# Kernel tuning notes

Hardware: AMD Instinct MI355X
Metric: run time of the kernel (lower is better)

The kernel has to match this reference:

```python
import jax, jax.numpy as jnp
import numpy as np
from jax import lax

H = 2048          # hidden_size
I = 1408          # moe_intermediate_size
E = 16            # n_routed_experts
K = 4             # num_experts_per_tok
N_SHARED = 2      # n_shared_experts
IS = I * N_SHARED # shared expert intermediate
B, S = 1, 1024


def setup_inputs() -> dict:
    key = jax.random.key(0)
    ks = jax.random.split(key, 8)
    scale = 0.02
    return {
        "hidden_states": jax.random.normal(ks[0], (B, S, H), dtype=jnp.float32),
        "gate_w": jax.random.normal(ks[1], (E, H), dtype=jnp.float32) * scale,  # MoEGate.weight
        "w_gate": jax.random.normal(ks[2], (E, H, I), dtype=jnp.float32) * scale,
        "w_up": jax.random.normal(ks[3], (E, H, I), dtype=jnp.float32) * scale,
        "w_down": jax.random.normal(ks[4], (E, I, H), dtype=jnp.float32) * scale,
        "sw_gate": jax.random.normal(ks[5], (H, IS), dtype=jnp.float32) * scale,
        "sw_up": jax.random.normal(ks[6], (H, IS), dtype=jnp.float32) * scale,
        "sw_down": jax.random.normal(ks[7], (IS, H), dtype=jnp.float32) * scale,
    }


def _moe_forward(hidden_states, gate_w, w_gate, w_up, w_down, sw_gate, sw_up, sw_down):
    bsz, seq_len, h = hidden_states.shape
    flat = hidden_states.reshape(-1, h)                # [T, H]
    T = flat.shape[0]

    # --- MoEGate: softmax scoring + top-k (norm_topk_prob=False) ---
    logits = flat @ gate_w.T                           # [T, E]
    scores = jax.nn.softmax(logits, axis=-1)
    topk_w, topk_idx = lax.top_k(scores, K)            # [T, K]

    # combine[t, e] = sum of top-k weights assigned to expert e (scatter of dispatch)
    combine = jnp.zeros((T, E), dtype=flat.dtype).at[
        jnp.arange(T)[:, None], topk_idx
    ].add(topk_w)                                      # [T, E]

    # --- routed experts: scan over experts, accumulate weighted SwiGLU MLP outputs ---
    def step(y, xs):
        wg, wu, wd, c = xs                             # [H,I], [H,I], [I,H], [T]
        out = (jax.nn.silu(flat @ wg) * (flat @ wu)) @ wd   # [T, H]
        return y + c[:, None] * out, None

    y, _ = lax.scan(step, jnp.zeros_like(flat), (w_gate, w_up, w_down, combine.T))

    # --- shared experts (always-on SwiGLU MLP with larger intermediate) ---
    shared = (jax.nn.silu(flat @ sw_gate) * (flat @ sw_up)) @ sw_down  # [T, H]

    return (y + shared).reshape(bsz, seq_len, h)


def reference(hidden_states, gate_w, w_gate, w_up, w_down, sw_gate, sw_up, sw_down):
    return _moe_forward(hidden_states, gate_w, w_gate, w_up, w_down,
                        sw_gate, sw_up, sw_down)
```

## Files before the change

kernel.cpp:

```cpp
#include <hip/hip_runtime.h>
#include <hip/hip_bf16.h>
#include <stdint.h>

#define T_TOK 1024
#define H_DIM 2048
#define I_DIM 1408
#define E_NUM 16
#define K_TOP 4
#define IS_DIM 2816
#define BK 64
#define BKP 72
#define BM 128
#define BN 128
#define NT_MAX 64

typedef __hip_bfloat16 bf;
typedef __attribute__((ext_vector_type(8))) __bf16 bf16x8;
typedef __attribute__((ext_vector_type(4))) float f32x4;

__device__ __forceinline__ void gload16(const void* g, void* l) {
  __builtin_amdgcn_global_load_lds((const __attribute__((address_space(1))) void*)g,
                                   (__attribute__((address_space(3))) void*)l, 16, 0, 0);
}

__global__ void cvt_x_kernel(const float* __restrict__ in, bf* __restrict__ out) {
  int i = blockIdx.x * blockDim.x + threadIdx.x;
  float4 v = reinterpret_cast<const float4*>(in)[i];
  int b = i * 4;
  out[b + 0] = __float2bfloat16(v.x);
  out[b + 1] = __float2bfloat16(v.y);
  out[b + 2] = __float2bfloat16(v.z);
  out[b + 3] = __float2bfloat16(v.w);
}

__global__ void gate_topk_kernel(const float* __restrict__ x, const float* __restrict__ gw,
                                 int* __restrict__ topk_idx, float* __restrict__ topk_w) {
  int t = blockIdx.x;
  int lane = threadIdx.x;
  float acc[E_NUM];
#pragma unroll
  for (int e = 0; e < E_NUM; e++) acc[e] = 0.f;
  const float* xt = x + (long)t * H_DIM;
  for (int h = lane; h < H_DIM; h += 64) {
    float xv = xt[h];
#pragma unroll
    for (int e = 0; e < E_NUM; e++) acc[e] += xv * gw[e * H_DIM + h];
  }
#pragma unroll
  for (int e = 0; e < E_NUM; e++) {
    float v = acc[e];
    for (int off = 32; off; off >>= 1) v += __shfl_xor(v, off, 64);
    acc[e] = v;
  }
  if (lane == 0) {
    float m = acc[0];
#pragma unroll
    for (int e = 1; e < E_NUM; e++) m = fmaxf(m, acc[e]);
    float sc[E_NUM];
    float s = 0.f;
#pragma unroll
    for (int e = 0; e < E_NUM; e++) { sc[e] = expf(acc[e] - m); s += sc[e]; }
    float inv = 1.f / s;
#pragma unroll
    for (int e = 0; e < E_NUM; e++) sc[e] *= inv;
    for (int k = 0; k < K_TOP; k++) {
      int bi = 0;
      float bv = sc[0];
      for (int e = 1; e < E_NUM; e++)
        if (sc[e] > bv) { bv = sc[e]; bi = e; }
      topk_idx[t * K_TOP + k] = bi;
      topk_w[t * K_TOP + k] = bv;
      sc[bi] = -1.f;
    }
  }
}

__global__ void build_lists_kernel(const int* __restrict__ topk_idx,
                                   int* __restrict__ rows, int* __restrict__ tile_expert,
                                   int* __restrict__ n_tiles) {
  __shared__ int cnt[E_NUM], cur[E_NUM], s_tb;
  int tid = threadIdx.x;
  if (tid < E_NUM) cnt[tid] = 0;
  __syncthreads();
  for (int p = tid; p < T_TOK * K_TOP; p += blockDim.x)
    atomicAdd(&cnt[topk_idx[p]], 1);
  __syncthreads();
  if (tid == 0) {
    int tb = 0;
    for (int e = 0; e < E_NUM; e++) {
      int nt = (cnt[e] + BM - 1) / BM;
      cur[e] = tb * BM;
      for (int j = 0; j < nt; j++) tile_expert[tb + j] = e;
      tb += nt;
    }
    for (int j = 0; j < 16; j++) tile_expert[tb + j] = 16 + (j >> 3);
    s_tb = tb;
    *n_tiles = tb + 16;
  }
  __syncthreads();
  int tb = s_tb;
  for (int r = tid; r < NT_MAX * BM; r += blockDim.x) rows[r] = -1;
  __syncthreads();
  for (int p = tid; p < T_TOK * K_TOP; p += blockDim.x) {
    int t = p >> 2, k = p & 3;
    int e = topk_idx[p];
    int slot = atomicAdd(&cur[e], 1);
    rows[slot] = t * 8 + k;
  }
  for (int idx = tid; idx < 16 * BM; idx += blockDim.x) {
    int j = idx >> 7, r = idx & 127;
    int t = (j & 7) * BM + r;
    rows[(tb + j) * BM + r] = t * 8 + 4 + (j >> 3);
  }
}

__launch_bounds__(256, 2)
__global__ void gemm_gateup_kernel(const bf* __restrict__ xb,
                                   const int* __restrict__ rows,
                                   const int* __restrict__ tile_expert,
                                   const int* __restrict__ n_tiles,
                                   const float* __restrict__ Wg,
                                   const float* __restrict__ Wu,
                                   const float* __restrict__ SWg,
                                   const float* __restrict__ SWu,
                                   bf* __restrict__ act) {
  int bid = blockIdx.x;
  const int q = (11 * NT_MAX) / 8;
  int idx = (bid & 7) * q + (bid >> 3);
  int x = idx / NT_MAX, rt = idx % NT_MAX;
  if (rt >= *n_tiles) return;
  int e = tile_expert[rt];
  bool sh = e >= 16;
  const float* gbase = sh ? (SWg + (e - 16) * I_DIM) : (Wg + (long)e * H_DIM * I_DIM);
  const float* ubase = sh ? (SWu + (e - 16) * I_DIM) : (Wu + (long)e * H_DIM * I_DIM);
  long bstride = sh ? IS_DIM : I_DIM;
  int i0 = x * BN;

  __shared__ bf lA[BM * BK];
  __shared__ bf lG[BN * BKP];
  __shared__ bf lU[BN * BKP];

  int tid = threadIdx.x, w = tid >> 6, lane = tid & 63;
  int l15 = lane & 15, lhi = lane >> 4;
  int kg = tid >> 5, ng = tid & 31;
  int sswz = (((lane & 7) ^ (lane >> 3)) * 8);
  int bco = (kg ^ (ng & 7)) * 8;

  const bf* asrc[4];
#pragma unroll
  for (int i = 0; i < 4; i++) {
    int rr = rt * BM + i * 32 + w * 8 + (lane >> 3);
    int p = rows[rr];
    int tok = (p >= 0) ? (p >> 3) : 0;
    asrc[i] = xb + (long)tok * H_DIM + sswz;
  }

  const float* pg = gbase + i0 + ng * 4 + (long)(kg * 8) * bstride;
  const float* pu = ubase + i0 + ng * 4 + (long)(kg * 8) * bstride;

  f32x4 accg[4][4], accu[4][4];
  f32x4 z4 = {0.f, 0.f, 0.f, 0.f};
#pragma unroll
  for (int m = 0; m < 4; m++)
#pragma unroll
    for (int n = 0; n < 4; n++) { accg[m][n] = z4; accu[m][n] = z4; }

  int wr = w >> 1, wc = w & 1;
  for (int kt = 0; kt < H_DIM; kt += BK) {
    float4 vg[8], vu[8];
    const float* pgk = pg + (long)kt * bstride;
    const float* puk = pu + (long)kt * bstride;
#pragma unroll
    for (int j = 0; j < 8; j++) {
      vg[j] = *reinterpret_cast<const float4*>(pgk + (long)j * bstride);
      vu[j] = *reinterpret_cast<const float4*>(puk + (long)j * bstride);
    }
    __syncthreads();
#pragma unroll
    for (int i = 0; i < 4; i++)
      gload16(asrc[i] + kt, lA + (i * 32 + w * 8) * BK);
#pragma unroll
    for (int c = 0; c < 4; c++) {
      union { bf16x8 v; bf s[8]; } og, ou;
#pragma unroll
      for (int j = 0; j < 8; j++) {
        og.s[j] = __float2bfloat16(((const float*)&vg[j])[c]);
        ou.s[j] = __float2bfloat16(((const float*)&vu[j])[c]);
      }
      *reinterpret_cast<bf16x8*>(lG + (ng * 4 + c) * BKP + bco) = og.v;
      *reinterpret_cast<bf16x8*>(lU + (ng * 4 + c) * BKP + bco) = ou.v;
    }
    __syncthreads();
#pragma unroll
    for (int kk = 0; kk < 2; kk++) {
      bf16x8 af[4];
#pragma unroll
      for (int m = 0; m < 4; m++)
        af[m] = *reinterpret_cast<const bf16x8*>(
            lA + (wr * 64 + m * 16 + l15) * BK + (((kk * 4 + lhi) ^ (l15 & 7)) * 8));
#pragma unroll
      for (int n = 0; n < 4; n++) {
        int nrow = wc * 64 + n * 16 + l15;
        int bch = ((kk * 4 + lhi) ^ ((nrow >> 2) & 7)) * 8;
        bf16x8 gf = *reinterpret_cast<const bf16x8*>(lG + nrow * BKP + bch);
        bf16x8 uf = *reinterpret_cast<const bf16x8*>(lU + nrow * BKP + bch);
#pragma unroll
        for (int m = 0; m < 4; m++) {
          accg[m][n] = __builtin_amdgcn_mfma_f32_16x16x32_bf16(af[m], gf, accg[m][n], 0, 0, 0);
          accu[m][n] = __builtin_amdgcn_mfma_f32_16x16x32_bf16(af[m], uf, accu[m][n], 0, 0, 0);
        }
      }
    }
  }

#pragma unroll
  for (int m = 0; m < 4; m++)
#pragma unroll
    for (int n = 0; n < 4; n++)
#pragma unroll
      for (int r2 = 0; r2 < 4; r2++) {
        float gv = accg[m][n][r2];
        float uv = accu[m][n][r2];
        float s = (gv / (1.f + __expf(-gv))) * uv;
        int row = rt * BM + wr * 64 + m * 16 + lhi * 4 + r2;
        int col = i0 + wc * 64 + n * 16 + l15;
        act[(long)row * I_DIM + col] = __float2bfloat16(s);
      }
}

__launch_bounds__(256, 3)
__global__ void gemm_down_kernel(const bf* __restrict__ A,
                                 const int* __restrict__ rows,
                                 const int* __restrict__ tile_expert,
                                 const int* __restrict__ n_tiles,
                                 const float* __restrict__ Wd,
                                 const float* __restrict__ SWd,
                                 bf* __restrict__ outp) {
  int bid = blockIdx.x;
  const int q = (16 * NT_MAX) / 8;
  int idx = (bid & 7) * q + (bid >> 3);
  int x = idx / NT_MAX, rt = idx % NT_MAX;
  if (rt >= *n_tiles) return;
  int e = tile_expert[rt];
  bool sh = e >= 16;
  const float* bbase = sh ? (SWd + (long)(e - 16) * I_DIM * H_DIM)
                          : (Wd + (long)e * I_DIM * H_DIM);
  int h0 = x * BN;

  __shared__ bf lA[BM * BK];
  __shared__ bf lB[BN * BKP];
  __shared__ int rowsl[BM];

  int tid = threadIdx.x, w = tid >> 6, lane = tid & 63;
  int l15 = lane & 15, lhi = lane >> 4;
  int kg = tid >> 5, ng = tid & 31;
  int sswz = (((lane & 7) ^ (lane >> 3)) * 8);
  int bco = (kg ^ (ng & 7)) * 8;
  if (tid < BM) rowsl[tid] = rows[rt * BM + tid];

  long aoff[4];
#pragma unroll
  for (int i = 0; i < 4; i++)
    aoff[i] = (long)(rt * BM + i * 32 + w * 8 + (lane >> 3)) * I_DIM + sswz;

  const float* pb = bbase + h0 + ng * 4 + (long)(kg * 8) * H_DIM;

  f32x4 acc[4][4];
  f32x4 z4 = {0.f, 0.f, 0.f, 0.f};
#pragma unroll
  for (int m = 0; m < 4; m++)
#pragma unroll
    for (int n = 0; n < 4; n++) acc[m][n] = z4;

  int wr = w >> 1, wc = w & 1;
  for (int kt = 0; kt < I_DIM; kt += BK) {
    float4 vb[8];
    const float* pbk = pb + (long)kt * H_DIM;
#pragma unroll
    for (int j = 0; j < 8; j++)
      vb[j] = *reinterpret_cast<const float4*>(pbk + (long)j * H_DIM);
    __syncthreads();
#pragma unroll
    for (int i = 0; i < 4; i++)
      gload16(A + aoff[i] + kt, lA + (i * 32 + w * 8) * BK);
#pragma unroll
    for (int c = 0; c < 4; c++) {
      union { bf16x8 v; bf s[8]; } ob;
#pragma unroll
      for (int j = 0; j < 8; j++)
        ob.s[j] = __float2bfloat16(((const float*)&vb[j])[c]);
      *reinterpret_cast<bf16x8*>(lB + (ng * 4 + c) * BKP + bco) = ob.v;
    }
    __syncthreads();
#pragma unroll
    for (int kk = 0; kk < 2; kk++) {
      bf16x8 af[4];
#pragma unroll
      for (int m = 0; m < 4; m++)
        af[m] = *reinterpret_cast<const bf16x8*>(
            lA + (wr * 64 + m * 16 + l15) * BK + (((kk * 4 + lhi) ^ (l15 & 7)) * 8));
#pragma unroll
      for (int n = 0; n < 4; n++) {
        int nrow = wc * 64 + n * 16 + l15;
        int bch = ((kk * 4 + lhi) ^ ((nrow >> 2) & 7)) * 8;
        bf16x8 bfr = *reinterpret_cast<const bf16x8*>(lB + nrow * BKP + bch);
#pragma unroll
        for (int m = 0; m < 4; m++)
          acc[m][n] = __builtin_amdgcn_mfma_f32_16x16x32_bf16(af[m], bfr, acc[m][n], 0, 0, 0);
      }
    }
  }

#pragma unroll
  for (int m = 0; m < 4; m++)
#pragma unroll
    for (int n = 0; n < 4; n++)
#pragma unroll
      for (int r2 = 0; r2 < 4; r2++) {
        int lrow = wr * 64 + m * 16 + lhi * 4 + r2;
        int col = h0 + wc * 64 + n * 16 + l15;
        int p = rowsl[lrow];
        if (p >= 0) outp[(long)p * H_DIM + col] = __float2bfloat16(acc[m][n][r2]);
      }
}

__global__ void combine_kernel(const bf* __restrict__ outp,
                               const float* __restrict__ topk_w,
                               float* __restrict__ out) {
  int idx = blockIdx.x * blockDim.x + threadIdx.x;
  int t = idx >> 11;
  int h = idx & 2047;
  const bf* base = outp + (long)t * 8 * H_DIM + h;
  float acc = __bfloat162float(base[4 * H_DIM]) + __bfloat162float(base[5 * H_DIM]);
#pragma unroll
  for (int k = 0; k < 4; k++)
    acc += topk_w[t * 4 + k] * __bfloat162float(base[(long)k * H_DIM]);
  out[idx] = acc;
}

extern "C" void kernel_launch(void* const* d_in, const int* in_sizes, int n_in,
                              void* d_out, int out_size, void* d_ws, size_t ws_size,
                              hipStream_t stream) {
  const float* x     = (const float*)d_in[0];
  const float* gw    = (const float*)d_in[1];
  const float* wgate = (const float*)d_in[2];
  const float* wup   = (const float*)d_in[3];
  const float* wdown = (const float*)d_in[4];
  const float* swg   = (const float*)d_in[5];
  const float* swu   = (const float*)d_in[6];
  const float* swd   = (const float*)d_in[7];
  float* out = (float*)d_out;

  char* ws = (char*)d_ws;
  size_t off = 0;
  auto alloc = [&](size_t bytes) {
    void* p = ws + off;
    off += (bytes + 255) & ~(size_t)255;
    return p;
  };

  bf* xb   = (bf*)alloc((size_t)T_TOK * H_DIM * 2);
  bf* act  = (bf*)alloc((size_t)NT_MAX * BM * I_DIM * 2);
  bf* outp = (bf*)alloc((size_t)T_TOK * 8 * H_DIM * 2);
  int*   topk_idx = (int*)alloc(T_TOK * K_TOP * 4);
  float* topk_w   = (float*)alloc(T_TOK * K_TOP * 4);
  int*   rowsbuf  = (int*)alloc(NT_MAX * BM * 4);
  int*   tile_exp = (int*)alloc(NT_MAX * 4);
  int*   n_tiles  = (int*)alloc(64);
  (void)ws_size; (void)in_sizes; (void)n_in; (void)out_size;

  hipLaunchKernelGGL(cvt_x_kernel, dim3(T_TOK * H_DIM / 1024), dim3(256), 0, stream, x, xb);
  hipLaunchKernelGGL(gate_topk_kernel, dim3(T_TOK), dim3(64), 0, stream, x, gw, topk_idx, topk_w);
  hipLaunchKernelGGL(build_lists_kernel, dim3(1), dim3(256), 0, stream, topk_idx, rowsbuf, tile_exp, n_tiles);

  hipLaunchKernelGGL(gemm_gateup_kernel, dim3((I_DIM / BN) * NT_MAX), dim3(256), 0, stream,
                     xb, rowsbuf, tile_exp, n_tiles, wgate, wup, swg, swu, act);
  hipLaunchKernelGGL(gemm_down_kernel, dim3((H_DIM / BN) * NT_MAX), dim3(256), 0, stream,
                     act, rowsbuf, tile_exp, n_tiles, wdown, swd, outp);

  hipLaunchKernelGGL(combine_kernel, dim3(T_TOK * H_DIM / 256), dim3(256), 0, stream,
                     outp, topk_w, out);
}
```

Baseline: 336.9 us.

## Double-buffer LDS in both expert GEMMs and narrow gate/up N tile

Both the gate/up and down GEMMs now keep two LDS stages. The next K-tile's global loads (fp32 weights into registers, bf16 activations via global_load_lds) are issued before the MFMAs on the current tile, with sched_barriers holding that order. This is meant to hide the load and conversion latency that the single-buffered loop left exposed. The gate/up kernel also halves its N tile to 64, doubling the grid, and the down kernel's occupancy hint drops from 3 to 2 because LDS use is now higher.

```diff
diff --git a/kernel.cpp b/kernel.cpp
--- a/kernel.cpp
+++ b/kernel.cpp
@@ -11,7 +11,6 @@
 #define BK 64
 #define BKP 72
 #define BM 128
-#define BN 128
 #define NT_MAX 64
 
 typedef __hip_bfloat16 bf;
@@ -125,26 +124,24 @@
                                    const float* __restrict__ SWu,
                                    bf* __restrict__ act) {
   int bid = blockIdx.x;
-  const int q = (11 * NT_MAX) / 8;
-  int idx = (bid & 7) * q + (bid >> 3);
-  int x = idx / NT_MAX, rt = idx % NT_MAX;
+  int idx = (bid & 7) * 176 + (bid >> 3);
+  int x = idx >> 6, rt = idx & 63;
   if (rt >= *n_tiles) return;
   int e = tile_expert[rt];
   bool sh = e >= 16;
   const float* gbase = sh ? (SWg + (e - 16) * I_DIM) : (Wg + (long)e * H_DIM * I_DIM);
   const float* ubase = sh ? (SWu + (e - 16) * I_DIM) : (Wu + (long)e * H_DIM * I_DIM);
   long bstride = sh ? IS_DIM : I_DIM;
-  int i0 = x * BN;
-
-  __shared__ bf lA[BM * BK];
-  __shared__ bf lG[BN * BKP];
-  __shared__ bf lU[BN * BKP];
+  int i0 = x * 64;
+
+  __shared__ bf lA[2][BM * BK];
+  __shared__ bf lB2[2][2][64 * BKP];
 
   int tid = threadIdx.x, w = tid >> 6, lane = tid & 63;
   int l15 = lane & 15, lhi = lane >> 4;
-  int kg = tid >> 5, ng = tid & 31;
+  int nq = tid & 15, mt = (tid >> 4) & 1, kg = tid >> 5;
   int sswz = (((lane & 7) ^ (lane >> 3)) * 8);
-  int bco = (kg ^ (ng & 7)) * 8;
+  int bco = (kg ^ (nq & 7)) * 8;
 
   const bf* asrc[4];
 #pragma unroll
@@ -155,80 +152,96 @@
     asrc[i] = xb + (long)tok * H_DIM + sswz;
   }
 
-  const float* pg = gbase + i0 + ng * 4 + (long)(kg * 8) * bstride;
-  const float* pu = ubase + i0 + ng * 4 + (long)(kg * 8) * bstride;
-
-  f32x4 accg[4][4], accu[4][4];
+  const float* psrc = (mt ? ubase : gbase) + i0 + nq * 4 + (long)(kg * 8) * bstride;
+
+  f32x4 accg[4][2], accu[4][2];
   f32x4 z4 = {0.f, 0.f, 0.f, 0.f};
 #pragma unroll
   for (int m = 0; m < 4; m++)
 #pragma unroll
-    for (int n = 0; n < 4; n++) { accg[m][n] = z4; accu[m][n] = z4; }
+    for (int n = 0; n < 2; n++) { accg[m][n] = z4; accu[m][n] = z4; }
 
   int wr = w >> 1, wc = w & 1;
-  for (int kt = 0; kt < H_DIM; kt += BK) {
-    float4 vg[8], vu[8];
-    const float* pgk = pg + (long)kt * bstride;
-    const float* puk = pu + (long)kt * bstride;
-#pragma unroll
-    for (int j = 0; j < 8; j++) {
-      vg[j] = *reinterpret_cast<const float4*>(pgk + (long)j * bstride);
-      vu[j] = *reinterpret_cast<const float4*>(puk + (long)j * bstride);
-    }
+  float4 v[8];
+
+#define GU_ISSUE(T, NB)                                                            \
+  {                                                                                \
+    const float* p_ = psrc + (long)(T) * BK * bstride;                             \
+    _Pragma("unroll") for (int j = 0; j < 8; j++)                                  \
+        v[j] = *reinterpret_cast<const float4*>(p_ + (long)j * bstride);           \
+    _Pragma("unroll") for (int i = 0; i < 4; i++)                                  \
+        gload16(asrc[i] + (T) * BK, &lA[NB][(i * 32 + w * 8) * BK]);               \
+  }
+
+#define GU_WRITE(NB)                                                               \
+  {                                                                                \
+    _Pragma("unroll") for (int c = 0; c < 4; c++) {                                \
+      union { bf16x8 vv; bf s[8]; } o;                                             \
+      _Pragma("unroll") for (int j = 0; j < 8; j++)                                \
+          o.s[j] = __float2bfloat16(((const float*)&v[j])[c]);                     \
+      *reinterpret_cast<bf16x8*>(&lB2[NB][mt][(nq * 4 + c) * BKP + bco]) = o.vv;   \
+    }                                                                              \
+  }
+
+#define GU_MFMA(CB)                                                                \
+  {                                                                                \
+    _Pragma("unroll") for (int kk = 0; kk < 2; kk++) {                             \
+      bf16x8 af[4];                                                                \
+      _Pragma("unroll") for (int m = 0; m < 4; m++)                                \
+          af[m] = *reinterpret_cast<const bf16x8*>(                                \
+              &lA[CB][(wr * 64 + m * 16 + l15) * BK + (((kk * 4 + lhi) ^ (l15 & 7)) * 8)]); \
+      _Pragma("unroll") for (int n = 0; n < 2; n++) {                              \
+        int nrow = wc * 32 + n * 16 + l15;                                         \
+        int bch = ((kk * 4 + lhi) ^ ((nrow >> 2) & 7)) * 8;                        \
+        bf16x8 gf = *reinterpret_cast<const bf16x8*>(&lB2[CB][0][nrow * BKP + bch]); \
+        bf16x8 uf = *reinterpret_cast<const bf16x8*>(&lB2[CB][1][nrow * BKP + bch]); \
+        _Pragma("unroll") for (int m = 0; m < 4; m++) {                            \
+          accg[m][n] = __builtin_amdgcn_mfma_f32_16x16x32_bf16(af[m], gf, accg[m][n], 0, 0, 0); \
+          accu[m][n] = __builtin_amdgcn_mfma_f32_16x16x32_bf16(af[m], uf, accu[m][n], 0, 0, 0); \
+        }                                                                          \
+      }                                                                            \
+    }                                                                              \
+  }
+
+  const int NT = H_DIM / BK;
+  GU_ISSUE(0, 0);
+  GU_WRITE(0);
+  __syncthreads();
+
+  for (int t = 0; t < NT; t += 2) {
+    GU_ISSUE(t + 1, 1);
+    __builtin_amdgcn_sched_barrier(0);
+    GU_MFMA(0);
+    __builtin_amdgcn_sched_barrier(0);
+    GU_WRITE(1);
     __syncthreads();
-#pragma unroll
-    for (int i = 0; i < 4; i++)
-      gload16(asrc[i] + kt, lA + (i * 32 + w * 8) * BK);
-#pragma unroll
-    for (int c = 0; c < 4; c++) {
-      union { bf16x8 v; bf s[8]; } og, ou;
-#pragma unroll
-      for (int j = 0; j < 8; j++) {
-        og.s[j] = __float2bfloat16(((const float*)&vg[j])[c]);
-        ou.s[j] = __float2bfloat16(((const float*)&vu[j])[c]);
-      }
-      *reinterpret_cast<bf16x8*>(lG + (ng * 4 + c) * BKP + bco) = og.v;
-      *reinterpret_cast<bf16x8*>(lU + (ng * 4 + c) * BKP + bco) = ou.v;
-    }
+    if (t + 2 < NT) GU_ISSUE(t + 2, 0);
+    __builtin_amdgcn_sched_barrier(0);
+    GU_MFMA(1);
+    __builtin_amdgcn_sched_barrier(0);
+    if (t + 2 < NT) GU_WRITE(0);
     __syncthreads();
-#pragma unroll
-    for (int kk = 0; kk < 2; kk++) {
-      bf16x8 af[4];
-#pragma unroll
-      for (int m = 0; m < 4; m++)
-        af[m] = *reinterpret_cast<const bf16x8*>(
-            lA + (wr * 64 + m * 16 + l15) * BK + (((kk * 4 + lhi) ^ (l15 & 7)) * 8));
-#pragma unroll
-      for (int n = 0; n < 4; n++) {
-        int nrow = wc * 64 + n * 16 + l15;
-        int bch = ((kk * 4 + lhi) ^ ((nrow >> 2) & 7)) * 8;
-        bf16x8 gf = *reinterpret_cast<const bf16x8*>(lG + nrow * BKP + bch);
-        bf16x8 uf = *reinterpret_cast<const bf16x8*>(lU + nrow * BKP + bch);
-#pragma unroll
-        for (int m = 0; m < 4; m++) {
-          accg[m][n] = __builtin_amdgcn_mfma_f32_16x16x32_bf16(af[m], gf, accg[m][n], 0, 0, 0);
-          accu[m][n] = __builtin_amdgcn_mfma_f32_16x16x32_bf16(af[m], uf, accu[m][n], 0, 0, 0);
-        }
-      }
-    }
-  }
+  }
+#undef GU_ISSUE
+#undef GU_WRITE
+#undef GU_MFMA
 
 #pragma unroll
   for (int m = 0; m < 4; m++)
 #pragma unroll
-    for (int n = 0; n < 4; n++)
+    for (int n = 0; n < 2; n++)
 #pragma unroll
       for (int r2 = 0; r2 < 4; r2++) {
         float gv = accg[m][n][r2];
         float uv = accu[m][n][r2];
         float s = (gv / (1.f + __expf(-gv))) * uv;
         int row = rt * BM + wr * 64 + m * 16 + lhi * 4 + r2;
-        int col = i0 + wc * 64 + n * 16 + l15;
+        int col = i0 + wc * 32 + n * 16 + l15;
         act[(long)row * I_DIM + col] = __float2bfloat16(s);
       }
 }
 
-__launch_bounds__(256, 3)
+__launch_bounds__(256, 2)
 __global__ void gemm_down_kernel(const bf* __restrict__ A,
                                  const int* __restrict__ rows,
                                  const int* __restrict__ tile_expert,
@@ -237,18 +250,17 @@
                                  const float* __restrict__ SWd,
                                  bf* __restrict__ outp) {
   int bid = blockIdx.x;
-  const int q = (16 * NT_MAX) / 8;
-  int idx = (bid & 7) * q + (bid >> 3);
-  int x = idx / NT_MAX, rt = idx % NT_MAX;
+  int idx = (bid & 7) * 128 + (bid >> 3);
+  int x = idx >> 6, rt = idx & 63;
   if (rt >= *n_tiles) return;
   int e = tile_expert[rt];
   bool sh = e >= 16;
   const float* bbase = sh ? (SWd + (long)(e - 16) * I_DIM * H_DIM)
                           : (Wd + (long)e * I_DIM * H_DIM);
-  int h0 = x * BN;
-
-  __shared__ bf lA[BM * BK];
-  __shared__ bf lB[BN * BKP];
+  int h0 = x * 128;
+
+  __shared__ bf lA[2][BM * BK];
+  __shared__ bf lB[2][128 * BKP];
   __shared__ int rowsl[BM];
 
   int tid = threadIdx.x, w = tid >> 6, lane = tid & 63;
@@ -258,12 +270,12 @@
   int bco = (kg ^ (ng & 7)) * 8;
   if (tid < BM) rowsl[tid] = rows[rt * BM + tid];
 
-  long aoff[4];
+  const bf* asrc[4];
 #pragma unroll
   for (int i = 0; i < 4; i++)
-    aoff[i] = (long)(rt * BM + i * 32 + w * 8 + (lane >> 3)) * I_DIM + sswz;
-
-  const float* pb = bbase + h0 + ng * 4 + (long)(kg * 8) * H_DIM;
+    asrc[i] = A + (long)(rt * BM + i * 32 + w * 8 + (lane >> 3)) * I_DIM + sswz;
+
+  const float* psrc = bbase + h0 + ng * 4 + (long)(kg * 8) * H_DIM;
 
   f32x4 acc[4][4];
   f32x4 z4 = {0.f, 0.f, 0.f, 0.f};
@@ -273,43 +285,66 @@
     for (int n = 0; n < 4; n++) acc[m][n] = z4;
 
   int wr = w >> 1, wc = w & 1;
-  for (int kt = 0; kt < I_DIM; kt += BK) {
-    float4 vb[8];
-    const float* pbk = pb + (long)kt * H_DIM;
-#pragma unroll
-    for (int j = 0; j < 8; j++)
-      vb[j] = *reinterpret_cast<const float4*>(pbk + (long)j * H_DIM);
+  float4 v[8];
+
+#define DN_ISSUE(T, NB)                                                            \
+  {                                                                                \
+    const float* p_ = psrc + (long)(T) * BK * H_DIM;                               \
+    _Pragma("unroll") for (int j = 0; j < 8; j++)                                  \
+        v[j] = *reinterpret_cast<const float4*>(p_ + (long)j * H_DIM);             \
+    _Pragma("unroll") for (int i = 0; i < 4; i++)                                  \
+        gload16(asrc[i] + (T) * BK, &lA[NB][(i * 32 + w * 8) * BK]);               \
+  }
+
+#define DN_WRITE(NB)                                                               \
+  {                                                                                \
+    _Pragma("unroll") for (int c = 0; c < 4; c++) {                                \
+      union { bf16x8 vv; bf s[8]; } o;                                             \
+      _Pragma("unroll") for (int j = 0; j < 8; j++)                                \
+          o.s[j] = __float2bfloat16(((const float*)&v[j])[c]);                     \
+      *reinterpret_cast<bf16x8*>(&lB[NB][(ng * 4 + c) * BKP + bco]) = o.vv;        \
+    }                                                                              \
+  }
+
+#define DN_MFMA(CB)                                                                \
+  {                                                                                \
+    _Pragma("unroll") for (int kk = 0; kk < 2; kk++) {                             \
+      bf16x8 af[4];                                                                \
+      _Pragma("unroll") for (int m = 0; m < 4; m++)                                \
+          af[m] = *reinterpret_cast<const bf16x8*>(                                \
+              &lA[CB][(wr * 64 + m * 16 + l15) * BK + (((kk * 4 + lhi) ^ (l15 & 7)) * 8)]); \
+      _Pragma("unroll") for (int n = 0; n < 4; n++) {                              \
+        int nrow = wc * 64 + n * 16 + l15;                                         \
+        int bch = ((kk * 4 + lhi) ^ ((nrow >> 2) & 7)) * 8;                        \
+        bf16x8 bfr = *reinterpret_cast<const bf16x8*>(&lB[CB][nrow * BKP + bch]);  \
+        _Pragma("unroll") for (int m = 0; m < 4; m++)                              \
+            acc[m][n] = __builtin_amdgcn_mfma_f32_16x16x32_bf16(af[m], bfr, acc[m][n], 0, 0, 0); \
+      }                                                                            \
+    }                                                                              \
+  }
+
+  const int NT = I_DIM / BK;
+  DN_ISSUE(0, 0);
+  DN_WRITE(0);
+  __syncthreads();
+
+  for (int t = 0; t < NT; t += 2) {
+    DN_ISSUE(t + 1, 1);
+    __builtin_amdgcn_sched_barrier(0);
+    DN_MFMA(0);
+    __builtin_amdgcn_sched_barrier(0);
+    DN_WRITE(1);
     __syncthreads();
-#pragma unroll
-    for (int i = 0; i < 4; i++)
-      gload16(A + aoff[i] + kt, lA + (i * 32 + w * 8) * BK);
-#pragma unroll
-    for (int c = 0; c < 4; c++) {
-      union { bf16x8 v; bf s[8]; } ob;
-#pragma unroll
-      for (int j = 0; j < 8; j++)
-        ob.s[j] = __float2bfloat16(((const float*)&vb[j])[c]);
-      *reinterpret_cast<bf16x8*>(lB + (ng * 4 + c) * BKP + bco) = ob.v;
-    }
+    if (t + 2 < NT) DN_ISSUE(t + 2, 0);
+    __builtin_amdgcn_sched_barrier(0);
+    DN_MFMA(1);
+    __builtin_amdgcn_sched_barrier(0);
+    if (t + 2 < NT) DN_WRITE(0);
     __syncthreads();
-#pragma unroll
-    for (int kk = 0; kk < 2; kk++) {
-      bf16x8 af[4];
-#pragma unroll
-      for (int m = 0; m < 4; m++)
-        af[m] = *reinterpret_cast<const bf16x8*>(
-            lA + (wr * 64 + m * 16 + l15) * BK + (((kk * 4 + lhi) ^ (l15 & 7)) * 8));
-#pragma unroll
-      for (int n = 0; n < 4; n++) {
-        int nrow = wc * 64 + n * 16 + l15;
-        int bch = ((kk * 4 + lhi) ^ ((nrow >> 2) & 7)) * 8;
-        bf16x8 bfr = *reinterpret_cast<const bf16x8*>(lB + nrow * BKP + bch);
-#pragma unroll
-        for (int m = 0; m < 4; m++)
-          acc[m][n] = __builtin_amdgcn_mfma_f32_16x16x32_bf16(af[m], bfr, acc[m][n], 0, 0, 0);
-      }
-    }
-  }
+  }
+#undef DN_ISSUE
+#undef DN_WRITE
+#undef DN_MFMA
 
 #pragma unroll
   for (int m = 0; m < 4; m++)
@@ -373,9 +408,9 @@
   hipLaunchKernelGGL(gate_topk_kernel, dim3(T_TOK), dim3(64), 0, stream, x, gw, topk_idx, topk_w);
   hipLaunchKernelGGL(build_lists_kernel, dim3(1), dim3(256), 0, stream, topk_idx, rowsbuf, tile_exp, n_tiles);
 
-  hipLaunchKernelGGL(gemm_gateup_kernel, dim3((I_DIM / BN) * NT_MAX), dim3(256), 0, stream,
+  hipLaunchKernelGGL(gemm_gateup_kernel, dim3((I_DIM / 64) * NT_MAX), dim3(256), 0, stream,
                      xb, rowsbuf, tile_exp, n_tiles, wgate, wup, swg, swu, act);
-  hipLaunchKernelGGL(gemm_down_kernel, dim3((H_DIM / BN) * NT_MAX), dim3(256), 0, stream,
+  hipLaunchKernelGGL(gemm_down_kernel, dim3((H_DIM / 128) * NT_MAX), dim3(256), 0, stream,
                      act, rowsbuf, tile_exp, n_tiles, wdown, swd, outp);
 
   hipLaunchKernelGGL(combine_kernel, dim3(T_TOK * H_DIM / 256), dim3(256), 0, stream,
```

Result: faster. 317.8 us (-5.7%).
